# Kernel optimization log

Measured on AMD Instinct MI355X. Metric: run time of the kernel, lower is better.

Reference implementation:

```python
import jax, jax.numpy as jnp
import numpy as np

N_NODES = 50000
N_FRAMES = 5
N_EDGES = 400000
H1, C1 = 8, 8
D_MODEL = 64
N_HEADS, HEAD_DIM = 4, 16
EPS = 1e-5


def _gat_conv(h_in, src, dst, W, a_src, a_dst, heads, ch):
    # PyG GATConv (eval mode): linear -> per-head attn logits -> leaky_relu ->
    # segment softmax over incoming edges of each dst node -> weighted scatter-add.
    N = h_in.shape[0]
    h = (h_in @ W.T).reshape(N, heads, ch)            # [N,H,C]
    a_s = (h * a_src).sum(-1)                          # [N,H]
    a_d = (h * a_dst).sum(-1)                          # [N,H]
    e = jax.nn.leaky_relu(a_s[src] + a_d[dst], negative_slope=0.2)  # [E,H]
    e_max = jax.ops.segment_max(e, dst, num_segments=N)             # [N,H]
    ex = jnp.exp(e - e_max[dst])
    denom = jax.ops.segment_sum(ex, dst, num_segments=N)
    alpha = ex / denom[dst]                            # [E,H]
    return jax.ops.segment_sum(h[src] * alpha[..., None], dst, num_segments=N)  # [N,H,C]


def _ln(x, w, b):
    m = x.mean(-1, keepdims=True)
    v = ((x - m) ** 2).mean(-1, keepdims=True)
    return (x - m) / jnp.sqrt(v + EPS) * w + b


def _forward(x, edge_index, W1, att_src1, att_dst1, b1, W2, att_src2, att_dst2, b2,
             tWqkv, tbqkv, tWo, tbo, tln1w, tln1b, tWff1, tbff1, tWff2, tbff2,
             tln2w, tln2b, Wh1, bh1, Wh2, bh2):
    loops = jnp.arange(N_NODES, dtype=edge_index.dtype)  # add_self_loops=True
    embs = []
    for f in range(N_FRAMES):  # fixed small frame window
        src = jnp.concatenate([edge_index[f, 0], loops])
        dst = jnp.concatenate([edge_index[f, 1], loops])
        h = _gat_conv(x[f], src, dst, W1, att_src1, att_dst1, H1, C1).reshape(N_NODES, H1 * C1) + b1
        h = jax.nn.elu(h)
        h = _gat_conv(h, src, dst, W2, att_src2, att_dst2, 1, D_MODEL)[:, 0] + b2  # concat=False, 1 head
        embs.append(h.mean(0))  # graph embedding [64]
    seq = jnp.stack(embs)[None]  # [1,5,64]
    scale = 1.0 / np.sqrt(HEAD_DIM)
    for l in range(tWqkv.shape[0]):  # post-norm TransformerEncoderLayer (eval, relu)
        B, S, _ = seq.shape
        qkv = seq @ tWqkv[l].T + tbqkv[l]
        q, k, v = jnp.split(qkv, 3, axis=-1)
        q = q.reshape(B, S, N_HEADS, HEAD_DIM)
        k = k.reshape(B, S, N_HEADS, HEAD_DIM)
        v = v.reshape(B, S, N_HEADS, HEAD_DIM)
        att = jax.nn.softmax(jnp.einsum('bqhd,bkhd->bhqk', q, k) * scale, axis=-1)
        o = jnp.einsum('bhqk,bkhd->bqhd', att, v).reshape(B, S, D_MODEL)
        seq = _ln(seq + o @ tWo[l].T + tbo[l], tln1w[l], tln1b[l])
        ff = jax.nn.relu(seq @ tWff1[l].T + tbff1[l]) @ tWff2[l].T + tbff2[l]
        seq = _ln(seq + ff, tln2w[l], tln2b[l])
    last = seq[:, -1, :]
    return jax.nn.relu(last @ Wh1.T + bh1) @ Wh2.T + bh2  # [1,2]


def setup_inputs():
    key = jax.random.key(0)
    ks = jax.random.split(key, 16)
    p = lambda i, shape, s=0.1: jax.random.normal(ks[i], shape, dtype=jnp.float32) * s
    return {
        'x': jax.random.normal(ks[0], (N_FRAMES, N_NODES, 13), dtype=jnp.float32),
        'edge_index': jax.random.randint(ks[1], (N_FRAMES, 2, N_EDGES), 0, N_NODES, dtype=jnp.int32),
        'W1': p(2, (64, 13)), 'att_src1': p(3, (H1, C1)), 'att_dst1': p(4, (H1, C1)), 'b1': jnp.zeros((64,), jnp.float32),
        'W2': p(5, (64, 64)), 'att_src2': p(6, (1, 64)), 'att_dst2': p(7, (1, 64)), 'b2': jnp.zeros((64,), jnp.float32),
        'tWqkv': p(8, (3, 192, 64)), 'tbqkv': jnp.zeros((3, 192), jnp.float32),
        'tWo': p(9, (3, 64, 64)), 'tbo': jnp.zeros((3, 64), jnp.float32),
        'tln1w': jnp.ones((3, 64), jnp.float32), 'tln1b': jnp.zeros((3, 64), jnp.float32),
        'tWff1': p(10, (3, 128, 64)), 'tbff1': jnp.zeros((3, 128), jnp.float32),
        'tWff2': p(11, (3, 64, 128)), 'tbff2': jnp.zeros((3, 64), jnp.float32),
        'tln2w': jnp.ones((3, 64), jnp.float32), 'tln2b': jnp.zeros((3, 64), jnp.float32),
        'Wh1': p(12, (32, 64)), 'bh1': jnp.zeros((32,), jnp.float32),
        'Wh2': p(13, (2, 32)), 'bh2': jnp.zeros((2,), jnp.float32),
    }


def reference(x, edge_index, W1, att_src1, att_dst1, b1, W2, att_src2, att_dst2, b2,
              tWqkv, tbqkv, tWo, tbo, tln1w, tln1b, tWff1, tbff1, tWff2, tbff2,
              tln2w, tln2b, Wh1, bh1, Wh2, bh2):
    return _forward(x, edge_index, W1, att_src1, att_dst1, b1, W2, att_src2, att_dst2, b2,
                    tWqkv, tbqkv, tWo, tbo, tln1w, tln1b, tWff1, tbff1, tWff2, tbff2,
                    tln2w, tln2b, Wh1, bh1, Wh2, bh2)
```

## Files before the change

### kernel.cpp

```cpp
#include <hip/hip_runtime.h>
#include <math.h>

#define NN_F 50000
#define NE_F 400000
#define BPF  768

__device__ __forceinline__ float lrelu02(float x) { return x > 0.f ? x : 0.2f * x; }
__device__ __forceinline__ float fexp(float x) { return __expf(x); }

__device__ __forceinline__ unsigned short f2bf(float f) {
  unsigned int u = __float_as_uint(f);
  u += 0x7fffu + ((u >> 16) & 1u);
  return (unsigned short)(u >> 16);
}
__device__ __forceinline__ float bf_lo(unsigned int u) { return __uint_as_float(u << 16); }
__device__ __forceinline__ float bf_hi(unsigned int u) { return __uint_as_float(u & 0xffff0000u); }
__device__ __forceinline__ unsigned int pack2(float a, float b) {
  return (unsigned int)f2bf(a) | ((unsigned int)f2bf(b) << 16);
}

typedef __attribute__((ext_vector_type(8))) short bfrag_t;
typedef __attribute__((ext_vector_type(4))) float facc_t;

__global__ void __launch_bounds__(256, 3)
k_rank_node1(const int* __restrict__ ei, int* __restrict__ deg,
             unsigned short* __restrict__ rank, int nFrames, int rankBlocks,
             const float* __restrict__ x, const float* __restrict__ W1,
             const float* __restrict__ attS, const float* __restrict__ attD,
             unsigned short* __restrict__ h1b, float* __restrict__ as1,
             float* __restrict__ ad1, int nNodes, int node1Blocks) {
  __shared__ float xbuf[4][16];
  if (blockIdx.x < rankBlocks) {
    int tid = blockIdx.x * blockDim.x + threadIdx.x;
    int T = (nFrames * NE_F) >> 2;
    if (tid >= T) return;
    int gd[4];
#pragma unroll
    for (int i = 0; i < 4; i++) {
      int e = tid + i * T;
      int f = e / NE_F, idx = e - f * NE_F;
      gd[i] = f * NN_F + ei[(size_t)f * 2 * NE_F + NE_F + idx];
    }
    int r[4];
#pragma unroll
    for (int i = 0; i < 4; i++) r[i] = atomicAdd(&deg[gd[i]], 1);
#pragma unroll
    for (int i = 0; i < 4; i++) rank[tid + i * T] = (unsigned short)r[i];
    return;
  }
  int bid = blockIdx.x - rankBlocks;
  int l = threadIdx.x & 63;
  int w = threadIdx.x >> 6;
  int wid = (bid * blockDim.x + threadIdx.x) >> 6;
  int nw = (node1Blocks * blockDim.x) >> 6;
  float4 wA = make_float4(W1[l * 13 + 0], W1[l * 13 + 1], W1[l * 13 + 2], W1[l * 13 + 3]);
  float4 wB = make_float4(W1[l * 13 + 4], W1[l * 13 + 5], W1[l * 13 + 6], W1[l * 13 + 7]);
  float4 wC = make_float4(W1[l * 13 + 8], W1[l * 13 + 9], W1[l * 13 + 10], W1[l * 13 + 11]);
  float4 wD = make_float4(W1[l * 13 + 12], 0.f, 0.f, 0.f);
  float aS = attS[l], aD = attD[l];
  const float4* xb = reinterpret_cast<const float4*>(xbuf[w]);
  for (int n = wid; n < nNodes; n += nw) {
    if (l < 16) xbuf[w][l] = (l < 13) ? x[(size_t)n * 13 + l] : 0.f;
    float4 x0 = xb[0], x1 = xb[1], x2 = xb[2], x3 = xb[3];
    float a0 = x0.x * wA.x, a1 = x0.y * wA.y, a2 = x0.z * wA.z, a3 = x0.w * wA.w;
    a0 = fmaf(x1.x, wB.x, a0); a1 = fmaf(x1.y, wB.y, a1);
    a2 = fmaf(x1.z, wB.z, a2); a3 = fmaf(x1.w, wB.w, a3);
    a0 = fmaf(x2.x, wC.x, a0); a1 = fmaf(x2.y, wC.y, a1);
    a2 = fmaf(x2.z, wC.z, a2); a3 = fmaf(x2.w, wC.w, a3);
    a0 = fmaf(x3.x, wD.x, a0);
    float acc = (a0 + a1) + (a2 + a3);
    h1b[(size_t)n * 64 + l] = f2bf(acc);
    float s = acc * aS, d = acc * aD;
#pragma unroll
    for (int off = 1; off < 8; off <<= 1) {
      s += __shfl_xor(s, off, 64);
      d += __shfl_xor(d, off, 64);
    }
    if ((l & 7) == 0) { as1[n * 8 + (l >> 3)] = s; ad1[n * 8 + (l >> 3)] = d; }
  }
}

__global__ void k_scan1(const int* __restrict__ deg, int* __restrict__ bsum, int nNodes) {
  __shared__ int part[256];
  int t = threadIdx.x;
  int i = blockIdx.x * 256 + t;
  part[t] = (i < nNodes) ? deg[i] : 0;
  __syncthreads();
  for (int off = 128; off > 0; off >>= 1) {
    if (t < off) part[t] += part[t + off];
    __syncthreads();
  }
  if (t == 0) bsum[blockIdx.x] = part[0];
}

__global__ void __launch_bounds__(1024)
k_scan2(const int* __restrict__ bsum, int* __restrict__ boff, int nblk) {
  __shared__ int part[1024];
  int t = threadIdx.x;
  part[t] = (t < nblk) ? bsum[t] : 0;
  __syncthreads();
  for (int off = 1; off < 1024; off <<= 1) {
    int v = (t >= off) ? part[t - off] : 0;
    __syncthreads();
    part[t] += v;
    __syncthreads();
  }
  if (t < nblk) boff[t] = part[t] - bsum[t];
}

__global__ void k_scan3(const int* __restrict__ deg, const int* __restrict__ boff,
                        int* __restrict__ rowptr, int nNodes, int nEdges) {
  __shared__ int part[256];
  int t = threadIdx.x;
  int i = blockIdx.x * 256 + t;
  int d = (i < nNodes) ? deg[i] : 0;
  part[t] = d;
  __syncthreads();
  for (int off = 1; off < 256; off <<= 1) {
    int v = (t >= off) ? part[t - off] : 0;
    __syncthreads();
    part[t] += v;
    __syncthreads();
  }
  if (i < nNodes) rowptr[i] = boff[blockIdx.x] + part[t] - d;
  if (blockIdx.x == 0 && t == 0) rowptr[nNodes] = nEdges;
}

__global__ void k_place(const int* __restrict__ ei, const int* __restrict__ rowptr,
                        const unsigned short* __restrict__ rank, int* __restrict__ csr,
                        int nFrames) {
  int tid = blockIdx.x * blockDim.x + threadIdx.x;
  int T = (nFrames * NE_F) >> 2;
  if (tid >= T) return;
#pragma unroll
  for (int i = 0; i < 4; i++) {
    int e = tid + i * T;
    int f = e / NE_F, idx = e - f * NE_F;
    const int* base = ei + (size_t)f * 2 * NE_F;
    int src = base[idx], dst = base[NE_F + idx];
    csr[rowptr[f * NN_F + dst] + (int)rank[e]] = f * NN_F + src;
  }
}

__global__ void __launch_bounds__(256)
k_agg1(const int* __restrict__ rowptr, const int* __restrict__ csr,
       const unsigned short* __restrict__ h1b, const float* __restrict__ as1,
       const float* __restrict__ ad1, unsigned short* __restrict__ out1b, int nNodes) {
  int t = threadIdx.x;
  int l = t & 63;
  int grp = l >> 3, q = l & 7;
  int n = ((blockIdx.x * blockDim.x + t) >> 6) * 8 + grp;
  if (n >= nNodes) return;
  float adv = ad1[n * 8 + q];
  float e0 = fexp(lrelu02(as1[n * 8 + q] + adv));
  uint4 pv = *reinterpret_cast<const uint4*>(h1b + (size_t)n * 64 + q * 8);
  float a0 = e0 * bf_lo(pv.x), a1 = e0 * bf_hi(pv.x);
  float a2 = e0 * bf_lo(pv.y), a3 = e0 * bf_hi(pv.y);
  float a4 = e0 * bf_lo(pv.z), a5 = e0 * bf_hi(pv.z);
  float a6 = e0 * bf_lo(pv.w), a7 = e0 * bf_hi(pv.w);
  float den = e0;
  int s0 = rowptr[n], s1 = rowptr[n + 1];
  int i = s0;
  for (; i + 2 <= s1; i += 2) {
    int src0 = csr[i], src1 = csr[i + 1];
    float ea = fexp(lrelu02(as1[src0 * 8 + q] + adv));
    float eb = fexp(lrelu02(as1[src1 * 8 + q] + adv));
    uint4 va = *reinterpret_cast<const uint4*>(h1b + (size_t)src0 * 64 + q * 8);
    uint4 vb = *reinterpret_cast<const uint4*>(h1b + (size_t)src1 * 64 + q * 8);
    a0 = fmaf(ea, bf_lo(va.x), a0); a1 = fmaf(ea, bf_hi(va.x), a1);
    a2 = fmaf(ea, bf_lo(va.y), a2); a3 = fmaf(ea, bf_hi(va.y), a3);
    a4 = fmaf(ea, bf_lo(va.z), a4); a5 = fmaf(ea, bf_hi(va.z), a5);
    a6 = fmaf(ea, bf_lo(va.w), a6); a7 = fmaf(ea, bf_hi(va.w), a7);
    a0 = fmaf(eb, bf_lo(vb.x), a0); a1 = fmaf(eb, bf_hi(vb.x), a1);
    a2 = fmaf(eb, bf_lo(vb.y), a2); a3 = fmaf(eb, bf_hi(vb.y), a3);
    a4 = fmaf(eb, bf_lo(vb.z), a4); a5 = fmaf(eb, bf_hi(vb.z), a5);
    a6 = fmaf(eb, bf_lo(vb.w), a6); a7 = fmaf(eb, bf_hi(vb.w), a7);
    den += ea + eb;
  }
  if (i < s1) {
    int src = csr[i];
    float e2 = fexp(lrelu02(as1[src * 8 + q] + adv));
    uint4 v = *reinterpret_cast<const uint4*>(h1b + (size_t)src * 64 + q * 8);
    a0 = fmaf(e2, bf_lo(v.x), a0); a1 = fmaf(e2, bf_hi(v.x), a1);
    a2 = fmaf(e2, bf_lo(v.y), a2); a3 = fmaf(e2, bf_hi(v.y), a3);
    a4 = fmaf(e2, bf_lo(v.z), a4); a5 = fmaf(e2, bf_hi(v.z), a5);
    a6 = fmaf(e2, bf_lo(v.w), a6); a7 = fmaf(e2, bf_hi(v.w), a7);
    den += e2;
  }
  float inv = 1.f / den;
  uint4 o;
  o.x = pack2(a0 * inv, a1 * inv);
  o.y = pack2(a2 * inv, a3 * inv);
  o.z = pack2(a4 * inv, a5 * inv);
  o.w = pack2(a6 * inv, a7 * inv);
  *reinterpret_cast<uint4*>(out1b + (size_t)n * 64 + q * 8) = o;
}

__global__ void __launch_bounds__(256)
k_node2(const unsigned short* __restrict__ out1b, const float* __restrict__ b1,
        const float* __restrict__ W2, const float* __restrict__ attS2,
        const float* __restrict__ attD2, unsigned short* __restrict__ gb,
        float* __restrict__ as2, float* __restrict__ ad2, int nNodes) {
  __shared__ unsigned short lg[4][16][72];
  int t = threadIdx.x, l = t & 63, w = t >> 6;
  int r16 = l & 15, g4 = l >> 4;

  bfrag_t bfr[8];
#pragma unroll
  for (int tt = 0; tt < 4; tt++) {
    const float* wrow = W2 + (tt * 16 + r16) * 64;
#pragma unroll
    for (int kc = 0; kc < 2; kc++) {
      float4 lo = *reinterpret_cast<const float4*>(wrow + kc * 32 + 4 * g4);
      float4 hi = *reinterpret_cast<const float4*>(wrow + kc * 32 + 16 + 4 * g4);
      union { unsigned short u[8]; bfrag_t v; } pk;
      pk.u[0] = f2bf(lo.x); pk.u[1] = f2bf(lo.y); pk.u[2] = f2bf(lo.z); pk.u[3] = f2bf(lo.w);
      pk.u[4] = f2bf(hi.x); pk.u[5] = f2bf(hi.y); pk.u[6] = f2bf(hi.z); pk.u[7] = f2bf(hi.w);
      bfr[tt * 2 + kc] = pk.v;
    }
  }
  float4 bias[2][2];
#pragma unroll
  for (int kc = 0; kc < 2; kc++)
#pragma unroll
    for (int h = 0; h < 2; h++)
      bias[kc][h] = *reinterpret_cast<const float4*>(b1 + kc * 32 + h * 16 + 4 * g4);
  float aSr0 = attS2[r16], aSr1 = attS2[16 + r16], aSr2 = attS2[32 + r16], aSr3 = attS2[48 + r16];
  float aDr0 = attD2[r16], aDr1 = attD2[16 + r16], aDr2 = attD2[32 + r16], aDr3 = attD2[48 + r16];

  int wid = (blockIdx.x * blockDim.x + t) >> 6;
  int nw = (gridDim.x * blockDim.x) >> 6;
  int ntiles = nNodes >> 4;
  for (int tile = wid; tile < ntiles; tile += nw) {
    int n0 = tile << 4;
    const unsigned short* arow = out1b + (size_t)(n0 + r16) * 64;
    facc_t acc0 = 0, acc1 = 0, acc2 = 0, acc3 = 0;
#pragma unroll
    for (int kc = 0; kc < 2; kc++) {
      union { unsigned short u[8]; bfrag_t v; } apk;
#pragma unroll
      for (int h = 0; h < 2; h++) {
        uint2 raw = *reinterpret_cast<const uint2*>(arow + kc * 32 + h * 16 + 4 * g4);
        float4 bb = bias[kc][h];
        float f0 = bf_lo(raw.x) + bb.x, f1 = bf_hi(raw.x) + bb.y;
        float f2 = bf_lo(raw.y) + bb.z, f3 = bf_hi(raw.y) + bb.w;
        f0 = f0 > 0.f ? f0 : (fexp(f0) - 1.f);
        f1 = f1 > 0.f ? f1 : (fexp(f1) - 1.f);
        f2 = f2 > 0.f ? f2 : (fexp(f2) - 1.f);
        f3 = f3 > 0.f ? f3 : (fexp(f3) - 1.f);
        apk.u[h * 4 + 0] = f2bf(f0); apk.u[h * 4 + 1] = f2bf(f1);
        apk.u[h * 4 + 2] = f2bf(f2); apk.u[h * 4 + 3] = f2bf(f3);
      }
      bfrag_t afr = apk.v;
      acc0 = __builtin_amdgcn_mfma_f32_16x16x32_bf16(afr, bfr[0 * 2 + kc], acc0, 0, 0, 0);
      acc1 = __builtin_amdgcn_mfma_f32_16x16x32_bf16(afr, bfr[1 * 2 + kc], acc1, 0, 0, 0);
      acc2 = __builtin_amdgcn_mfma_f32_16x16x32_bf16(afr, bfr[2 * 2 + kc], acc2, 0, 0, 0);
      acc3 = __builtin_amdgcn_mfma_f32_16x16x32_bf16(afr, bfr[3 * 2 + kc], acc3, 0, 0, 0);
    }
    float ps0 = acc0[0] * aSr0 + acc1[0] * aSr1 + acc2[0] * aSr2 + acc3[0] * aSr3;
    float ps1 = acc0[1] * aSr0 + acc1[1] * aSr1 + acc2[1] * aSr2 + acc3[1] * aSr3;
    float ps2 = acc0[2] * aSr0 + acc1[2] * aSr1 + acc2[2] * aSr2 + acc3[2] * aSr3;
    float ps3 = acc0[3] * aSr0 + acc1[3] * aSr1 + acc2[3] * aSr2 + acc3[3] * aSr3;
    float pd0 = acc0[0] * aDr0 + acc1[0] * aDr1 + acc2[0] * aDr2 + acc3[0] * aDr3;
    float pd1 = acc0[1] * aDr0 + acc1[1] * aDr1 + acc2[1] * aDr2 + acc3[1] * aDr3;
    float pd2 = acc0[2] * aDr0 + acc1[2] * aDr1 + acc2[2] * aDr2 + acc3[2] * aDr3;
    float pd3 = acc0[3] * aDr0 + acc1[3] * aDr1 + acc2[3] * aDr2 + acc3[3] * aDr3;
#pragma unroll
    for (int off = 1; off < 16; off <<= 1) {
      ps0 += __shfl_xor(ps0, off, 64); ps1 += __shfl_xor(ps1, off, 64);
      ps2 += __shfl_xor(ps2, off, 64); ps3 += __shfl_xor(ps3, off, 64);
      pd0 += __shfl_xor(pd0, off, 64); pd1 += __shfl_xor(pd1, off, 64);
      pd2 += __shfl_xor(pd2, off, 64); pd3 += __shfl_xor(pd3, off, 64);
    }
    if (r16 == 0) {
      *reinterpret_cast<float4*>(as2 + n0 + g4 * 4) = make_float4(ps0, ps1, ps2, ps3);
      *reinterpret_cast<float4*>(ad2 + n0 + g4 * 4) = make_float4(pd0, pd1, pd2, pd3);
    }
#pragma unroll
    for (int r = 0; r < 4; r++) {
      lg[w][g4 * 4 + r][0 * 16 + r16] = f2bf(acc0[r]);
      lg[w][g4 * 4 + r][1 * 16 + r16] = f2bf(acc1[r]);
      lg[w][g4 * 4 + r][2 * 16 + r16] = f2bf(acc2[r]);
      lg[w][g4 * 4 + r][3 * 16 + r16] = f2bf(acc3[r]);
    }
    asm volatile("s_waitcnt lgkmcnt(0)" ::: "memory");
    int row = l >> 3, c = l & 7;
    uint4 v0 = *reinterpret_cast<const uint4*>(&lg[w][row][c * 8]);
    uint4 v1 = *reinterpret_cast<const uint4*>(&lg[w][8 + row][c * 8]);
    *reinterpret_cast<uint4*>(gb + (size_t)(n0 + row) * 64 + c * 8) = v0;
    *reinterpret_cast<uint4*>(gb + (size_t)(n0 + 8 + row) * 64 + c * 8) = v1;
  }
}

__global__ void __launch_bounds__(256)
k_agg2mean(const int* __restrict__ rowptr, const int* __restrict__ csr,
           const unsigned short* __restrict__ gtab, const float* __restrict__ as2,
           const float* __restrict__ ad2, float* __restrict__ emb) {
  __shared__ float part[32][64];
  int t = threadIdx.x;
  int w = t >> 6, l = t & 63;
  int grp = l >> 3, q = l & 7;
  int f = blockIdx.x / BPF;
  int gf = (blockIdx.x - f * BPF) * 32 + w * 8 + grp;
  const int stride = BPF * 32;
  float m0 = 0.f, m1 = 0.f, m2 = 0.f, m3 = 0.f, m4 = 0.f, m5 = 0.f, m6 = 0.f, m7 = 0.f;
  for (int j = gf; j < NN_F; j += stride) {
    int n = f * NN_F + j;
    float adv = ad2[n];
    float e0 = fexp(lrelu02(as2[n] + adv));
    uint4 pv = *reinterpret_cast<const uint4*>(gtab + (size_t)n * 64 + q * 8);
    float a0 = e0 * bf_lo(pv.x), a1 = e0 * bf_hi(pv.x);
    float a2 = e0 * bf_lo(pv.y), a3 = e0 * bf_hi(pv.y);
    float a4 = e0 * bf_lo(pv.z), a5 = e0 * bf_hi(pv.z);
    float a6 = e0 * bf_lo(pv.w), a7 = e0 * bf_hi(pv.w);
    float den = e0;
    int s0 = rowptr[n], s1 = rowptr[n + 1];
    int i = s0;
    for (; i + 2 <= s1; i += 2) {
      int src0 = csr[i], src1 = csr[i + 1];
      float ea = fexp(lrelu02(as2[src0] + adv));
      float eb = fexp(lrelu02(as2[src1] + adv));
      uint4 va = *reinterpret_cast<const uint4*>(gtab + (size_t)src0 * 64 + q * 8);
      uint4 vb = *reinterpret_cast<const uint4*>(gtab + (size_t)src1 * 64 + q * 8);
      a0 = fmaf(ea, bf_lo(va.x), a0); a1 = fmaf(ea, bf_hi(va.x), a1);
      a2 = fmaf(ea, bf_lo(va.y), a2); a3 = fmaf(ea, bf_hi(va.y), a3);
      a4 = fmaf(ea, bf_lo(va.z), a4); a5 = fmaf(ea, bf_hi(va.z), a5);
      a6 = fmaf(ea, bf_lo(va.w), a6); a7 = fmaf(ea, bf_hi(va.w), a7);
      a0 = fmaf(eb, bf_lo(vb.x), a0); a1 = fmaf(eb, bf_hi(vb.x), a1);
      a2 = fmaf(eb, bf_lo(vb.y), a2); a3 = fmaf(eb, bf_hi(vb.y), a3);
      a4 = fmaf(eb, bf_lo(vb.z), a4); a5 = fmaf(eb, bf_hi(vb.z), a5);
      a6 = fmaf(eb, bf_lo(vb.w), a6); a7 = fmaf(eb, bf_hi(vb.w), a7);
      den += ea + eb;
    }
    if (i < s1) {
      int src = csr[i];
      float e2 = fexp(lrelu02(as2[src] + adv));
      uint4 v = *reinterpret_cast<const uint4*>(gtab + (size_t)src * 64 + q * 8);
      a0 = fmaf(e2, bf_lo(v.x), a0); a1 = fmaf(e2, bf_hi(v.x), a1);
      a2 = fmaf(e2, bf_lo(v.y), a2); a3 = fmaf(e2, bf_hi(v.y), a3);
      a4 = fmaf(e2, bf_lo(v.z), a4); a5 = fmaf(e2, bf_hi(v.z), a5);
      a6 = fmaf(e2, bf_lo(v.w), a6); a7 = fmaf(e2, bf_hi(v.w), a7);
      den += e2;
    }
    float inv = 1.f / den;
    m0 = fmaf(a0, inv, m0); m1 = fmaf(a1, inv, m1);
    m2 = fmaf(a2, inv, m2); m3 = fmaf(a3, inv, m3);
    m4 = fmaf(a4, inv, m4); m5 = fmaf(a5, inv, m5);
    m6 = fmaf(a6, inv, m6); m7 = fmaf(a7, inv, m7);
  }
  float4* pr = reinterpret_cast<float4*>(&part[w * 8 + grp][q * 8]);
  pr[0] = make_float4(m0, m1, m2, m3);
  pr[1] = make_float4(m4, m5, m6, m7);
  __syncthreads();
  if (t < 64) {
    float s = 0.f;
#pragma unroll
    for (int r = 0; r < 32; r++) s += part[r][t];
    atomicAdd(&emb[f * 64 + t], s * (1.0f / NN_F));
  }
}

__device__ __forceinline__ float grp16_reduce(float p) {
#pragma unroll
  for (int off = 1; off < 16; off <<= 1) p += __shfl_xor(p, off, 64);
  return p;
}

__global__ void __launch_bounds__(1024)
k_transformer(const float* __restrict__ emb, const float* __restrict__ b2,
              const float* __restrict__ Wqkv, const float* __restrict__ bqkv,
              const float* __restrict__ Wo, const float* __restrict__ bo,
              const float* __restrict__ ln1w, const float* __restrict__ ln1b,
              const float* __restrict__ Wff1, const float* __restrict__ bff1,
              const float* __restrict__ Wff2, const float* __restrict__ bff2,
              const float* __restrict__ ln2w, const float* __restrict__ ln2b,
              const float* __restrict__ Wh1, const float* __restrict__ bh1,
              const float* __restrict__ Wh2, const float* __restrict__ bh2,
              float* __restrict__ out) {
  __shared__ float seq[5][64];
  __shared__ float qkv[5][192];
  __shared__ float att[4][5][5];
  __shared__ float aob[5][64];
  __shared__ float ffb[5][128];
  __shared__ float tmp[5][64];
  __shared__ float hid[32];
  int t = threadIdx.x;
  int l = t & 63, w = t >> 6;
  int g = l >> 4, q = l & 15;

  if (t < 320) seq[t >> 6][t & 63] = emb[t] + b2[t & 63];
  __syncthreads();

  for (int ly = 0; ly < 3; ly++) {
    const float* Wq  = Wqkv + ly * 12288; const float* bq  = bqkv + ly * 192;
    const float* Wol = Wo   + ly * 4096;  const float* bol = bo   + ly * 64;
    const float* w1  = ln1w + ly * 64;    const float* bb1 = ln1b + ly * 64;
    const float* Wf1 = Wff1 + ly * 8192;  const float* bf1 = bff1 + ly * 128;
    const float* Wf2 = Wff2 + ly * 8192;  const float* bf2 = bff2 + ly * 64;
    const float* w2  = ln2w + ly * 64;    const float* bb2 = ln2b + ly * 64;

    for (int o = w * 4 + g; o < 960; o += 64) {
      int s = o / 192, j = o - s * 192;
      float4 wv = *reinterpret_cast<const float4*>(&Wq[j * 64 + q * 4]);
      float4 xv = *reinterpret_cast<const float4*>(&seq[s][q * 4]);
      float p = wv.x * xv.x + wv.y * xv.y + wv.z * xv.z + wv.w * xv.w;
      p = grp16_reduce(p);
      if (q == 0) qkv[s][j] = p + bq[j];
    }
    __syncthreads();

    if (t < 100) {
      int hh = t / 25, qs = (t / 5) % 5, ks = t % 5;
      float acc = 0.f;
      for (int d = 0; d < 16; d++)
        acc = fmaf(qkv[qs][hh * 16 + d], qkv[ks][64 + hh * 16 + d], acc);
      att[hh][qs][ks] = acc * 0.25f;
    }
    __syncthreads();
    if (t < 20) {
      int hh = t / 5, qs = t % 5;
      float m = att[hh][qs][0];
      for (int k2 = 1; k2 < 5; k2++) m = fmaxf(m, att[hh][qs][k2]);
      float ss = 0.f;
      for (int k2 = 0; k2 < 5; k2++) { float v = expf(att[hh][qs][k2] - m); att[hh][qs][k2] = v; ss += v; }
      float inv = 1.f / ss;
      for (int k2 = 0; k2 < 5; k2++) att[hh][qs][k2] *= inv;
    }
    __syncthreads();

    if (t < 320) {
      int s = t >> 6, j = t & 63, hh = j >> 4;
      float acc = 0.f;
      for (int k2 = 0; k2 < 5; k2++) acc = fmaf(att[hh][s][k2], qkv[k2][128 + j], acc);
      aob[s][j] = acc;
    }
    __syncthreads();

    for (int o = w * 4 + g; o < 320; o += 64) {
      int s = o >> 6, c = o & 63;
      float4 wv = *reinterpret_cast<const float4*>(&Wol[c * 64 + q * 4]);
      float4 xv = *reinterpret_cast<const float4*>(&aob[s][q * 4]);
      float p = wv.x * xv.x + wv.y * xv.y + wv.z * xv.z + wv.w * xv.w;
      p = grp16_reduce(p);
      if (q == 0) tmp[s][c] = seq[s][c] + p + bol[c];
    }
    __syncthreads();

    if (w < 5) {
      float v = tmp[w][l];
      float s1 = v, s2 = v * v;
#pragma unroll
      for (int off = 1; off < 64; off <<= 1) {
        s1 += __shfl_xor(s1, off, 64);
        s2 += __shfl_xor(s2, off, 64);
      }
      float m = s1 * (1.f / 64.f);
      float var = s2 * (1.f / 64.f) - m * m;
      float inv = 1.f / sqrtf(var + 1e-5f);
      seq[w][l] = (v - m) * inv * w1[l] + bb1[l];
    }
    __syncthreads();

    for (int o = w * 4 + g; o < 640; o += 64) {
      int s = o >> 7, j = o & 127;
      float4 wv = *reinterpret_cast<const float4*>(&Wf1[j * 64 + q * 4]);
      float4 xv = *reinterpret_cast<const float4*>(&seq[s][q * 4]);
      float p = wv.x * xv.x + wv.y * xv.y + wv.z * xv.z + wv.w * xv.w;
      p = grp16_reduce(p);
      if (q == 0) ffb[s][j] = fmaxf(p + bf1[j], 0.f);
    }
    __syncthreads();

    for (int o = w * 4 + g; o < 320; o += 64) {
      int s = o >> 6, c = o & 63;
      float4 wa = *reinterpret_cast<const float4*>(&Wf2[c * 128 + q * 8]);
      float4 wb = *reinterpret_cast<const float4*>(&Wf2[c * 128 + q * 8 + 4]);
      float4 xa = *reinterpret_cast<const float4*>(&ffb[s][q * 8]);
      float4 xb = *reinterpret_cast<const float4*>(&ffb[s][q * 8 + 4]);
      float p = wa.x * xa.x + wa.y * xa.y + wa.z * xa.z + wa.w * xa.w
              + wb.x * xb.x + wb.y * xb.y + wb.z * xb.z + wb.w * xb.w;
      p = grp16_reduce(p);
      if (q == 0) tmp[s][c] = seq[s][c] + p + bf2[c];
    }
    __syncthreads();

    if (w < 5) {
      float v = tmp[w][l];
      float s1 = v, s2 = v * v;
#pragma unroll
      for (int off = 1; off < 64; off <<= 1) {
        s1 += __shfl_xor(s1, off, 64);
        s2 += __shfl_xor(s2, off, 64);
      }
      float m = s1 * (1.f / 64.f);
      float var = s2 * (1.f / 64.f) - m * m;
      float inv = 1.f / sqrtf(var + 1e-5f);
      seq[w][l] = (v - m) * inv * w2[l] + bb2[l];
    }
    __syncthreads();
  }

  for (int o = w * 4 + g; o < 32; o += 64) {
    float4 wv = *reinterpret_cast<const float4*>(&Wh1[o * 64 + q * 4]);
    float4 xv = *reinterpret_cast<const float4*>(&seq[4][q * 4]);
    float p = wv.x * xv.x + wv.y * xv.y + wv.z * xv.z + wv.w * xv.w;
    p = grp16_reduce(p);
    if (q == 0) hid[o] = fmaxf(p + bh1[o], 0.f);
  }
  __syncthreads();
  if (t < 2) {
    float acc = bh2[t];
    for (int j = 0; j < 32; j++) acc = fmaf(hid[j], Wh2[t * 32 + j], acc);
    out[t] = acc;
  }
}

extern "C" void kernel_launch(void* const* d_in, const int* in_sizes, int n_in,
                              void* d_out, int out_size, void* d_ws, size_t ws_size,
                              hipStream_t stream) {
  const float* x     = (const float*)d_in[0];
  const int*   ei    = (const int*)d_in[1];
  const float* W1    = (const float*)d_in[2];
  const float* attS1 = (const float*)d_in[3];
  const float* attD1 = (const float*)d_in[4];
  const float* b1    = (const float*)d_in[5];
  const float* W2    = (const float*)d_in[6];
  const float* attS2 = (const float*)d_in[7];
  const float* attD2 = (const float*)d_in[8];
  const float* b2    = (const float*)d_in[9];
  const float* tWqkv = (const float*)d_in[10];
  const float* tbqkv = (const float*)d_in[11];
  const float* tWo   = (const float*)d_in[12];
  const float* tbo   = (const float*)d_in[13];
  const float* tln1w = (const float*)d_in[14];
  const float* tln1b = (const float*)d_in[15];
  const float* tWff1 = (const float*)d_in[16];
  const float* tbff1 = (const float*)d_in[17];
  const float* tWff2 = (const float*)d_in[18];
  const float* tbff2 = (const float*)d_in[19];
  const float* tln2w = (const float*)d_in[20];
  const float* tln2b = (const float*)d_in[21];
  const float* Wh1   = (const float*)d_in[22];
  const float* bh1   = (const float*)d_in[23];
  const float* Wh2   = (const float*)d_in[24];
  const float* bh2   = (const float*)d_in[25];
  float* out = (float*)d_out;

  auto need_bytes = [](int F) -> size_t {
    size_t NT = (size_t)F * NN_F, ET = (size_t)F * NE_F;
    return (NT * 18 + 320) * 4 + (NT * 192 + ET) * 2 + (NT * 2 + 1 + 2048 + ET) * 4;
  };
  const int F = (ws_size >= need_bytes(5)) ? 5 : 1;
  const int NT = F * NN_F, ET = F * NE_F;

  float* ws  = (float*)d_ws;
  float* as1 = ws;
  float* ad1 = as1 + (size_t)NT * 8;
  float* as2 = ad1 + (size_t)NT * 8;
  float* ad2 = as2 + NT;
  float* emb = ad2 + NT;
  unsigned short* h1b   = (unsigned short*)(emb + 320);
  unsigned short* gb    = h1b + (size_t)NT * 64;
  unsigned short* out1b = gb + (size_t)NT * 64;
  int* deg    = (int*)(out1b + (size_t)NT * 64);
  int* rowptr = deg + NT;
  int* bsum   = rowptr + NT + 1;
  int* boff   = bsum + 1024;
  unsigned short* rank = (unsigned short*)(boff + 1024);
  int* csr    = (int*)(rank + ET);

  (void)hipMemsetAsync(emb, 0, 320 * sizeof(float), stream);

  const int nblk = (NT + 255) / 256;
  const int edge4Blocks = ((ET >> 2) + 255) / 256;
  const int agg1Blocks = (NT / 8 + 3) / 4;
  const int node1Blocks = 2048;
  const int node2Blocks = 1024;

  for (int f0 = 0; f0 < 5; f0 += F) {
    const float* xf = x + (size_t)f0 * NN_F * 13;
    const int* eif  = ei + (size_t)f0 * 2 * NE_F;

    (void)hipMemsetAsync(deg, 0, NT * sizeof(int), stream);
    k_rank_node1<<<edge4Blocks + node1Blocks, 256, 0, stream>>>(
        eif, deg, rank, F, edge4Blocks,
        xf, W1, attS1, attD1, h1b, as1, ad1, NT, node1Blocks);
    k_scan1<<<nblk, 256, 0, stream>>>(deg, bsum, NT);
    k_scan2<<<1, 1024, 0, stream>>>(bsum, boff, nblk);
    k_scan3<<<nblk, 256, 0, stream>>>(deg, boff, rowptr, NT, ET);
    k_place<<<edge4Blocks, 256, 0, stream>>>(eif, rowptr, rank, csr, F);

    k_agg1<<<agg1Blocks, 256, 0, stream>>>(rowptr, csr, h1b, as1, ad1, out1b, NT);
    k_node2<<<node2Blocks, 256, 0, stream>>>(out1b, b1, W2, attS2, attD2, gb, as2, ad2, NT);
    k_agg2mean<<<F * BPF, 256, 0, stream>>>(rowptr, csr, gb, as2, ad2, emb + f0 * 64);
  }

  k_transformer<<<1, 1024, 0, stream>>>(emb, b2, tWqkv, tbqkv, tWo, tbo, tln1w, tln1b,
                                        tWff1, tbff1, tWff2, tbff2, tln2w, tln2b,
                                        Wh1, bh1, Wh2, bh2, out);
}
```

Before: 360.5 us.

## Fuse layer-1 aggregation with layer-2 linear via LDS and unroll edge loops by four

Merges the first GAT aggregation kernel with the second layer's linear/attention projection kernel. Each block aggregates 32 nodes, applies the bias and ELU, stages the bf16 rows in shared memory, and then two waves run the MFMA projection, so the out1b buffer no longer round-trips through global memory and one launch is dropped. The edge gather loops in both aggregation kernels are also unrolled from two to four edges to put more loads in flight. In exchange, only two of the four waves do the MFMA stage, every chunk needs two block barriers, and the larger unroll raises register pressure.

```diff
diff --git a/kernel.cpp b/kernel.cpp
--- a/kernel.cpp
+++ b/kernel.cpp
@@ -142,67 +142,58 @@
   }
 }
 
+#define EDGE_ACC(tab, srcv, attarr, attidx)                          \
+  {                                                                  \
+    float e2 = fexp(lrelu02(attarr[attidx] + adv));                  \
+    uint4 v = *reinterpret_cast<const uint4*>(tab + (size_t)(srcv) * 64 + q * 8); \
+    a0 = fmaf(e2, bf_lo(v.x), a0); a1 = fmaf(e2, bf_hi(v.x), a1);    \
+    a2 = fmaf(e2, bf_lo(v.y), a2); a3 = fmaf(e2, bf_hi(v.y), a3);    \
+    a4 = fmaf(e2, bf_lo(v.z), a4); a5 = fmaf(e2, bf_hi(v.z), a5);    \
+    a6 = fmaf(e2, bf_lo(v.w), a6); a7 = fmaf(e2, bf_hi(v.w), a7);    \
+    den += e2;                                                       \
+  }
+
+#define EDGE_LOOP4(tab, attexpr_a, attexpr_b, attexpr_c, attexpr_d)  \
+  for (; i + 4 <= s1; i += 4) {                                      \
+    int sa = csr[i], sb = csr[i + 1], sc = csr[i + 2], sd = csr[i + 3]; \
+    float ea = fexp(lrelu02((attexpr_a) + adv));                     \
+    float eb = fexp(lrelu02((attexpr_b) + adv));                     \
+    float ec = fexp(lrelu02((attexpr_c) + adv));                     \
+    float ed = fexp(lrelu02((attexpr_d) + adv));                     \
+    uint4 va = *reinterpret_cast<const uint4*>(tab + (size_t)sa * 64 + q * 8); \
+    uint4 vb = *reinterpret_cast<const uint4*>(tab + (size_t)sb * 64 + q * 8); \
+    uint4 vc = *reinterpret_cast<const uint4*>(tab + (size_t)sc * 64 + q * 8); \
+    uint4 vd = *reinterpret_cast<const uint4*>(tab + (size_t)sd * 64 + q * 8); \
+    a0 = fmaf(ea, bf_lo(va.x), a0); a1 = fmaf(ea, bf_hi(va.x), a1);  \
+    a2 = fmaf(ea, bf_lo(va.y), a2); a3 = fmaf(ea, bf_hi(va.y), a3);  \
+    a4 = fmaf(ea, bf_lo(va.z), a4); a5 = fmaf(ea, bf_hi(va.z), a5);  \
+    a6 = fmaf(ea, bf_lo(va.w), a6); a7 = fmaf(ea, bf_hi(va.w), a7);  \
+    a0 = fmaf(eb, bf_lo(vb.x), a0); a1 = fmaf(eb, bf_hi(vb.x), a1);  \
+    a2 = fmaf(eb, bf_lo(vb.y), a2); a3 = fmaf(eb, bf_hi(vb.y), a3);  \
+    a4 = fmaf(eb, bf_lo(vb.z), a4); a5 = fmaf(eb, bf_hi(vb.z), a5);  \
+    a6 = fmaf(eb, bf_lo(vb.w), a6); a7 = fmaf(eb, bf_hi(vb.w), a7);  \
+    a0 = fmaf(ec, bf_lo(vc.x), a0); a1 = fmaf(ec, bf_hi(vc.x), a1);  \
+    a2 = fmaf(ec, bf_lo(vc.y), a2); a3 = fmaf(ec, bf_hi(vc.y), a3);  \
+    a4 = fmaf(ec, bf_lo(vc.z), a4); a5 = fmaf(ec, bf_hi(vc.z), a5);  \
+    a6 = fmaf(ec, bf_lo(vc.w), a6); a7 = fmaf(ec, bf_hi(vc.w), a7);  \
+    a0 = fmaf(ed, bf_lo(vd.x), a0); a1 = fmaf(ed, bf_hi(vd.x), a1);  \
+    a2 = fmaf(ed, bf_lo(vd.y), a2); a3 = fmaf(ed, bf_hi(vd.y), a3);  \
+    a4 = fmaf(ed, bf_lo(vd.z), a4); a5 = fmaf(ed, bf_hi(vd.z), a5);  \
+    a6 = fmaf(ed, bf_lo(vd.w), a6); a7 = fmaf(ed, bf_hi(vd.w), a7);  \
+    den += (ea + eb) + (ec + ed);                                    \
+  }
+
 __global__ void __launch_bounds__(256)
-k_agg1(const int* __restrict__ rowptr, const int* __restrict__ csr,
-       const unsigned short* __restrict__ h1b, const float* __restrict__ as1,
-       const float* __restrict__ ad1, unsigned short* __restrict__ out1b, int nNodes) {
-  int t = threadIdx.x;
-  int l = t & 63;
+k_agg1node2(const int* __restrict__ rowptr, const int* __restrict__ csr,
+            const unsigned short* __restrict__ h1b, const float* __restrict__ as1,
+            const float* __restrict__ ad1, const float* __restrict__ b1,
+            const float* __restrict__ W2, const float* __restrict__ attS2,
+            const float* __restrict__ attD2, unsigned short* __restrict__ gb,
+            float* __restrict__ as2, float* __restrict__ ad2, int nNodes) {
+  __shared__ unsigned short lout[32][68];
+  __shared__ unsigned short lg[2][16][72];
+  int t = threadIdx.x, l = t & 63, w = t >> 6;
   int grp = l >> 3, q = l & 7;
-  int n = ((blockIdx.x * blockDim.x + t) >> 6) * 8 + grp;
-  if (n >= nNodes) return;
-  float adv = ad1[n * 8 + q];
-  float e0 = fexp(lrelu02(as1[n * 8 + q] + adv));
-  uint4 pv = *reinterpret_cast<const uint4*>(h1b + (size_t)n * 64 + q * 8);
-  float a0 = e0 * bf_lo(pv.x), a1 = e0 * bf_hi(pv.x);
-  float a2 = e0 * bf_lo(pv.y), a3 = e0 * bf_hi(pv.y);
-  float a4 = e0 * bf_lo(pv.z), a5 = e0 * bf_hi(pv.z);
-  float a6 = e0 * bf_lo(pv.w), a7 = e0 * bf_hi(pv.w);
-  float den = e0;
-  int s0 = rowptr[n], s1 = rowptr[n + 1];
-  int i = s0;
-  for (; i + 2 <= s1; i += 2) {
-    int src0 = csr[i], src1 = csr[i + 1];
-    float ea = fexp(lrelu02(as1[src0 * 8 + q] + adv));
-    float eb = fexp(lrelu02(as1[src1 * 8 + q] + adv));
-    uint4 va = *reinterpret_cast<const uint4*>(h1b + (size_t)src0 * 64 + q * 8);
-    uint4 vb = *reinterpret_cast<const uint4*>(h1b + (size_t)src1 * 64 + q * 8);
-    a0 = fmaf(ea, bf_lo(va.x), a0); a1 = fmaf(ea, bf_hi(va.x), a1);
-    a2 = fmaf(ea, bf_lo(va.y), a2); a3 = fmaf(ea, bf_hi(va.y), a3);
-    a4 = fmaf(ea, bf_lo(va.z), a4); a5 = fmaf(ea, bf_hi(va.z), a5);
-    a6 = fmaf(ea, bf_lo(va.w), a6); a7 = fmaf(ea, bf_hi(va.w), a7);
-    a0 = fmaf(eb, bf_lo(vb.x), a0); a1 = fmaf(eb, bf_hi(vb.x), a1);
-    a2 = fmaf(eb, bf_lo(vb.y), a2); a3 = fmaf(eb, bf_hi(vb.y), a3);
-    a4 = fmaf(eb, bf_lo(vb.z), a4); a5 = fmaf(eb, bf_hi(vb.z), a5);
-    a6 = fmaf(eb, bf_lo(vb.w), a6); a7 = fmaf(eb, bf_hi(vb.w), a7);
-    den += ea + eb;
-  }
-  if (i < s1) {
-    int src = csr[i];
-    float e2 = fexp(lrelu02(as1[src * 8 + q] + adv));
-    uint4 v = *reinterpret_cast<const uint4*>(h1b + (size_t)src * 64 + q * 8);
-    a0 = fmaf(e2, bf_lo(v.x), a0); a1 = fmaf(e2, bf_hi(v.x), a1);
-    a2 = fmaf(e2, bf_lo(v.y), a2); a3 = fmaf(e2, bf_hi(v.y), a3);
-    a4 = fmaf(e2, bf_lo(v.z), a4); a5 = fmaf(e2, bf_hi(v.z), a5);
-    a6 = fmaf(e2, bf_lo(v.w), a6); a7 = fmaf(e2, bf_hi(v.w), a7);
-    den += e2;
-  }
-  float inv = 1.f / den;
-  uint4 o;
-  o.x = pack2(a0 * inv, a1 * inv);
-  o.y = pack2(a2 * inv, a3 * inv);
-  o.z = pack2(a4 * inv, a5 * inv);
-  o.w = pack2(a6 * inv, a7 * inv);
-  *reinterpret_cast<uint4*>(out1b + (size_t)n * 64 + q * 8) = o;
-}
-
-__global__ void __launch_bounds__(256)
-k_node2(const unsigned short* __restrict__ out1b, const float* __restrict__ b1,
-        const float* __restrict__ W2, const float* __restrict__ attS2,
-        const float* __restrict__ attD2, unsigned short* __restrict__ gb,
-        float* __restrict__ as2, float* __restrict__ ad2, int nNodes) {
-  __shared__ unsigned short lg[4][16][72];
-  int t = threadIdx.x, l = t & 63, w = t >> 6;
   int r16 = l & 15, g4 = l >> 4;
 
   bfrag_t bfr[8];
@@ -219,76 +210,99 @@
       bfr[tt * 2 + kc] = pk.v;
     }
   }
-  float4 bias[2][2];
-#pragma unroll
-  for (int kc = 0; kc < 2; kc++)
-#pragma unroll
-    for (int h = 0; h < 2; h++)
-      bias[kc][h] = *reinterpret_cast<const float4*>(b1 + kc * 32 + h * 16 + 4 * g4);
+  float4 bA = *reinterpret_cast<const float4*>(b1 + q * 8);
+  float4 bB = *reinterpret_cast<const float4*>(b1 + q * 8 + 4);
   float aSr0 = attS2[r16], aSr1 = attS2[16 + r16], aSr2 = attS2[32 + r16], aSr3 = attS2[48 + r16];
   float aDr0 = attD2[r16], aDr1 = attD2[16 + r16], aDr2 = attD2[32 + r16], aDr3 = attD2[48 + r16];
 
-  int wid = (blockIdx.x * blockDim.x + t) >> 6;
-  int nw = (gridDim.x * blockDim.x) >> 6;
-  int ntiles = nNodes >> 4;
-  for (int tile = wid; tile < ntiles; tile += nw) {
-    int n0 = tile << 4;
-    const unsigned short* arow = out1b + (size_t)(n0 + r16) * 64;
-    facc_t acc0 = 0, acc1 = 0, acc2 = 0, acc3 = 0;
-#pragma unroll
-    for (int kc = 0; kc < 2; kc++) {
-      union { unsigned short u[8]; bfrag_t v; } apk;
-#pragma unroll
-      for (int h = 0; h < 2; h++) {
-        uint2 raw = *reinterpret_cast<const uint2*>(arow + kc * 32 + h * 16 + 4 * g4);
-        float4 bb = bias[kc][h];
-        float f0 = bf_lo(raw.x) + bb.x, f1 = bf_hi(raw.x) + bb.y;
-        float f2 = bf_lo(raw.y) + bb.z, f3 = bf_hi(raw.y) + bb.w;
-        f0 = f0 > 0.f ? f0 : (fexp(f0) - 1.f);
-        f1 = f1 > 0.f ? f1 : (fexp(f1) - 1.f);
-        f2 = f2 > 0.f ? f2 : (fexp(f2) - 1.f);
-        f3 = f3 > 0.f ? f3 : (fexp(f3) - 1.f);
-        apk.u[h * 4 + 0] = f2bf(f0); apk.u[h * 4 + 1] = f2bf(f1);
-        apk.u[h * 4 + 2] = f2bf(f2); apk.u[h * 4 + 3] = f2bf(f3);
-      }
-      bfrag_t afr = apk.v;
-      acc0 = __builtin_amdgcn_mfma_f32_16x16x32_bf16(afr, bfr[0 * 2 + kc], acc0, 0, 0, 0);
-      acc1 = __builtin_amdgcn_mfma_f32_16x16x32_bf16(afr, bfr[1 * 2 + kc], acc1, 0, 0, 0);
-      acc2 = __builtin_amdgcn_mfma_f32_16x16x32_bf16(afr, bfr[2 * 2 + kc], acc2, 0, 0, 0);
-      acc3 = __builtin_amdgcn_mfma_f32_16x16x32_bf16(afr, bfr[3 * 2 + kc], acc3, 0, 0, 0);
-    }
-    float ps0 = acc0[0] * aSr0 + acc1[0] * aSr1 + acc2[0] * aSr2 + acc3[0] * aSr3;
-    float ps1 = acc0[1] * aSr0 + acc1[1] * aSr1 + acc2[1] * aSr2 + acc3[1] * aSr3;
-    float ps2 = acc0[2] * aSr0 + acc1[2] * aSr1 + acc2[2] * aSr2 + acc3[2] * aSr3;
-    float ps3 = acc0[3] * aSr0 + acc1[3] * aSr1 + acc2[3] * aSr2 + acc3[3] * aSr3;
-    float pd0 = acc0[0] * aDr0 + acc1[0] * aDr1 + acc2[0] * aDr2 + acc3[0] * aDr3;
-    float pd1 = acc0[1] * aDr0 + acc1[1] * aDr1 + acc2[1] * aDr2 + acc3[1] * aDr3;
-    float pd2 = acc0[2] * aDr0 + acc1[2] * aDr1 + acc2[2] * aDr2 + acc3[2] * aDr3;
-    float pd3 = acc0[3] * aDr0 + acc1[3] * aDr1 + acc2[3] * aDr2 + acc3[3] * aDr3;
-#pragma unroll
-    for (int off = 1; off < 16; off <<= 1) {
-      ps0 += __shfl_xor(ps0, off, 64); ps1 += __shfl_xor(ps1, off, 64);
-      ps2 += __shfl_xor(ps2, off, 64); ps3 += __shfl_xor(ps3, off, 64);
-      pd0 += __shfl_xor(pd0, off, 64); pd1 += __shfl_xor(pd1, off, 64);
-      pd2 += __shfl_xor(pd2, off, 64); pd3 += __shfl_xor(pd3, off, 64);
-    }
-    if (r16 == 0) {
-      *reinterpret_cast<float4*>(as2 + n0 + g4 * 4) = make_float4(ps0, ps1, ps2, ps3);
-      *reinterpret_cast<float4*>(ad2 + n0 + g4 * 4) = make_float4(pd0, pd1, pd2, pd3);
-    }
-#pragma unroll
-    for (int r = 0; r < 4; r++) {
-      lg[w][g4 * 4 + r][0 * 16 + r16] = f2bf(acc0[r]);
-      lg[w][g4 * 4 + r][1 * 16 + r16] = f2bf(acc1[r]);
-      lg[w][g4 * 4 + r][2 * 16 + r16] = f2bf(acc2[r]);
-      lg[w][g4 * 4 + r][3 * 16 + r16] = f2bf(acc3[r]);
-    }
-    asm volatile("s_waitcnt lgkmcnt(0)" ::: "memory");
-    int row = l >> 3, c = l & 7;
-    uint4 v0 = *reinterpret_cast<const uint4*>(&lg[w][row][c * 8]);
-    uint4 v1 = *reinterpret_cast<const uint4*>(&lg[w][8 + row][c * 8]);
-    *reinterpret_cast<uint4*>(gb + (size_t)(n0 + row) * 64 + c * 8) = v0;
-    *reinterpret_cast<uint4*>(gb + (size_t)(n0 + 8 + row) * 64 + c * 8) = v1;
+  int nchunks = (nNodes + 31) >> 5;
+  for (int c = blockIdx.x; c < nchunks; c += gridDim.x) {
+    int n0 = c << 5;
+    int n = n0 + w * 8 + grp;
+    if (n < nNodes) {
+      float adv = ad1[n * 8 + q];
+      float e0 = fexp(lrelu02(as1[n * 8 + q] + adv));
+      uint4 pv = *reinterpret_cast<const uint4*>(h1b + (size_t)n * 64 + q * 8);
+      float a0 = e0 * bf_lo(pv.x), a1 = e0 * bf_hi(pv.x);
+      float a2 = e0 * bf_lo(pv.y), a3 = e0 * bf_hi(pv.y);
+      float a4 = e0 * bf_lo(pv.z), a5 = e0 * bf_hi(pv.z);
+      float a6 = e0 * bf_lo(pv.w), a7 = e0 * bf_hi(pv.w);
+      float den = e0;
+      int s0 = rowptr[n], s1 = rowptr[n + 1];
+      int i = s0;
+      EDGE_LOOP4(h1b, as1[sa * 8 + q], as1[sb * 8 + q], as1[sc * 8 + q], as1[sd * 8 + q])
+      for (; i < s1; i++) {
+        int src = csr[i];
+        EDGE_ACC(h1b, src, as1, src * 8 + q)
+      }
+      float inv = 1.f / den;
+      float h0 = a0 * inv + bA.x, h1 = a1 * inv + bA.y;
+      float h2 = a2 * inv + bA.z, h3 = a3 * inv + bA.w;
+      float h4 = a4 * inv + bB.x, h5 = a5 * inv + bB.y;
+      float h6 = a6 * inv + bB.z, h7 = a7 * inv + bB.w;
+      h0 = h0 > 0.f ? h0 : (fexp(h0) - 1.f);
+      h1 = h1 > 0.f ? h1 : (fexp(h1) - 1.f);
+      h2 = h2 > 0.f ? h2 : (fexp(h2) - 1.f);
+      h3 = h3 > 0.f ? h3 : (fexp(h3) - 1.f);
+      h4 = h4 > 0.f ? h4 : (fexp(h4) - 1.f);
+      h5 = h5 > 0.f ? h5 : (fexp(h5) - 1.f);
+      h6 = h6 > 0.f ? h6 : (fexp(h6) - 1.f);
+      h7 = h7 > 0.f ? h7 : (fexp(h7) - 1.f);
+      uint4 o;
+      o.x = pack2(h0, h1); o.y = pack2(h2, h3);
+      o.z = pack2(h4, h5); o.w = pack2(h6, h7);
+      *reinterpret_cast<uint4*>(&lout[w * 8 + grp][q * 8]) = o;
+    }
+    __syncthreads();
+    int tb = n0 + w * 16;
+    if (w < 2 && tb < nNodes) {
+      const unsigned short* arow = &lout[w * 16 + r16][0];
+      facc_t acc0 = 0, acc1 = 0, acc2 = 0, acc3 = 0;
+#pragma unroll
+      for (int kc = 0; kc < 2; kc++) {
+        union { uint2 d[2]; bfrag_t v; } apk;
+        apk.d[0] = *reinterpret_cast<const uint2*>(arow + kc * 32 + 4 * g4);
+        apk.d[1] = *reinterpret_cast<const uint2*>(arow + kc * 32 + 16 + 4 * g4);
+        bfrag_t afr = apk.v;
+        acc0 = __builtin_amdgcn_mfma_f32_16x16x32_bf16(afr, bfr[0 * 2 + kc], acc0, 0, 0, 0);
+        acc1 = __builtin_amdgcn_mfma_f32_16x16x32_bf16(afr, bfr[1 * 2 + kc], acc1, 0, 0, 0);
+        acc2 = __builtin_amdgcn_mfma_f32_16x16x32_bf16(afr, bfr[2 * 2 + kc], acc2, 0, 0, 0);
+        acc3 = __builtin_amdgcn_mfma_f32_16x16x32_bf16(afr, bfr[3 * 2 + kc], acc3, 0, 0, 0);
+      }
+      float ps0 = acc0[0] * aSr0 + acc1[0] * aSr1 + acc2[0] * aSr2 + acc3[0] * aSr3;
+      float ps1 = acc0[1] * aSr0 + acc1[1] * aSr1 + acc2[1] * aSr2 + acc3[1] * aSr3;
+      float ps2 = acc0[2] * aSr0 + acc1[2] * aSr1 + acc2[2] * aSr2 + acc3[2] * aSr3;
+      float ps3 = acc0[3] * aSr0 + acc1[3] * aSr1 + acc2[3] * aSr2 + acc3[3] * aSr3;
+      float pd0 = acc0[0] * aDr0 + acc1[0] * aDr1 + acc2[0] * aDr2 + acc3[0] * aDr3;
+      float pd1 = acc0[1] * aDr0 + acc1[1] * aDr1 + acc2[1] * aDr2 + acc3[1] * aDr3;
+      float pd2 = acc0[2] * aDr0 + acc1[2] * aDr1 + acc2[2] * aDr2 + acc3[2] * aDr3;
+      float pd3 = acc0[3] * aDr0 + acc1[3] * aDr1 + acc2[3] * aDr2 + acc3[3] * aDr3;
+#pragma unroll
+      for (int off = 1; off < 16; off <<= 1) {
+        ps0 += __shfl_xor(ps0, off, 64); ps1 += __shfl_xor(ps1, off, 64);
+        ps2 += __shfl_xor(ps2, off, 64); ps3 += __shfl_xor(ps3, off, 64);
+        pd0 += __shfl_xor(pd0, off, 64); pd1 += __shfl_xor(pd1, off, 64);
+        pd2 += __shfl_xor(pd2, off, 64); pd3 += __shfl_xor(pd3, off, 64);
+      }
+      if (r16 == 0) {
+        *reinterpret_cast<float4*>(as2 + tb + g4 * 4) = make_float4(ps0, ps1, ps2, ps3);
+        *reinterpret_cast<float4*>(ad2 + tb + g4 * 4) = make_float4(pd0, pd1, pd2, pd3);
+      }
+#pragma unroll
+      for (int r = 0; r < 4; r++) {
+        lg[w][g4 * 4 + r][0 * 16 + r16] = f2bf(acc0[r]);
+        lg[w][g4 * 4 + r][1 * 16 + r16] = f2bf(acc1[r]);
+        lg[w][g4 * 4 + r][2 * 16 + r16] = f2bf(acc2[r]);
+        lg[w][g4 * 4 + r][3 * 16 + r16] = f2bf(acc3[r]);
+      }
+      asm volatile("s_waitcnt lgkmcnt(0)" ::: "memory");
+      int row = l >> 3, cc = l & 7;
+      uint4 v0 = *reinterpret_cast<const uint4*>(&lg[w][row][cc * 8]);
+      uint4 v1 = *reinterpret_cast<const uint4*>(&lg[w][8 + row][cc * 8]);
+      *reinterpret_cast<uint4*>(gb + (size_t)(tb + row) * 64 + cc * 8) = v0;
+      *reinterpret_cast<uint4*>(gb + (size_t)(tb + 8 + row) * 64 + cc * 8) = v1;
+    }
+    __syncthreads();
   }
 }
 
@@ -316,31 +330,10 @@
     float den = e0;
     int s0 = rowptr[n], s1 = rowptr[n + 1];
     int i = s0;
-    for (; i + 2 <= s1; i += 2) {
-      int src0 = csr[i], src1 = csr[i + 1];
-      float ea = fexp(lrelu02(as2[src0] + adv));
-      float eb = fexp(lrelu02(as2[src1] + adv));
-      uint4 va = *reinterpret_cast<const uint4*>(gtab + (size_t)src0 * 64 + q * 8);
-      uint4 vb = *reinterpret_cast<const uint4*>(gtab + (size_t)src1 * 64 + q * 8);
-      a0 = fmaf(ea, bf_lo(va.x), a0); a1 = fmaf(ea, bf_hi(va.x), a1);
-      a2 = fmaf(ea, bf_lo(va.y), a2); a3 = fmaf(ea, bf_hi(va.y), a3);
-      a4 = fmaf(ea, bf_lo(va.z), a4); a5 = fmaf(ea, bf_hi(va.z), a5);
-      a6 = fmaf(ea, bf_lo(va.w), a6); a7 = fmaf(ea, bf_hi(va.w), a7);
-      a0 = fmaf(eb, bf_lo(vb.x), a0); a1 = fmaf(eb, bf_hi(vb.x), a1);
-      a2 = fmaf(eb, bf_lo(vb.y), a2); a3 = fmaf(eb, bf_hi(vb.y), a3);
-      a4 = fmaf(eb, bf_lo(vb.z), a4); a5 = fmaf(eb, bf_hi(vb.z), a5);
-      a6 = fmaf(eb, bf_lo(vb.w), a6); a7 = fmaf(eb, bf_hi(vb.w), a7);
-      den += ea + eb;
-    }
-    if (i < s1) {
+    EDGE_LOOP4(gtab, as2[sa], as2[sb], as2[sc], as2[sd])
+    for (; i < s1; i++) {
       int src = csr[i];
-      float e2 = fexp(lrelu02(as2[src] + adv));
-      uint4 v = *reinterpret_cast<const uint4*>(gtab + (size_t)src * 64 + q * 8);
-      a0 = fmaf(e2, bf_lo(v.x), a0); a1 = fmaf(e2, bf_hi(v.x), a1);
-      a2 = fmaf(e2, bf_lo(v.y), a2); a3 = fmaf(e2, bf_hi(v.y), a3);
-      a4 = fmaf(e2, bf_lo(v.z), a4); a5 = fmaf(e2, bf_hi(v.z), a5);
-      a6 = fmaf(e2, bf_lo(v.w), a6); a7 = fmaf(e2, bf_hi(v.w), a7);
-      den += e2;
+      EDGE_ACC(gtab, src, as2, src)
     }
     float inv = 1.f / den;
     m0 = fmaf(a0, inv, m0); m1 = fmaf(a1, inv, m1);
@@ -548,7 +541,7 @@
 
   auto need_bytes = [](int F) -> size_t {
     size_t NT = (size_t)F * NN_F, ET = (size_t)F * NE_F;
-    return (NT * 18 + 320) * 4 + (NT * 192 + ET) * 2 + (NT * 2 + 1 + 2048 + ET) * 4;
+    return (NT * 18 + 320) * 4 + (NT * 128 + ET) * 2 + (NT * 2 + 1 + 2048 + ET) * 4;
   };
   const int F = (ws_size >= need_bytes(5)) ? 5 : 1;
   const int NT = F * NN_F, ET = F * NE_F;
@@ -559,10 +552,9 @@
   float* as2 = ad1 + (size_t)NT * 8;
   float* ad2 = as2 + NT;
   float* emb = ad2 + NT;
-  unsigned short* h1b   = (unsigned short*)(emb + 320);
-  unsigned short* gb    = h1b + (size_t)NT * 64;
-  unsigned short* out1b = gb + (size_t)NT * 64;
-  int* deg    = (int*)(out1b + (size_t)NT * 64);
+  unsigned short* h1b = (unsigned short*)(emb + 320);
+  unsigned short* gb  = h1b + (size_t)NT * 64;
+  int* deg    = (int*)(gb + (size_t)NT * 64);
   int* rowptr = deg + NT;
   int* bsum   = rowptr + NT + 1;
   int* boff   = bsum + 1024;
@@ -573,9 +565,8 @@
 
   const int nblk = (NT + 255) / 256;
   const int edge4Blocks = ((ET >> 2) + 255) / 256;
-  const int agg1Blocks = (NT / 8 + 3) / 4;
   const int node1Blocks = 2048;
-  const int node2Blocks = 1024;
+  const int aggFusedBlocks = 2048;
 
   for (int f0 = 0; f0 < 5; f0 += F) {
     const float* xf = x + (size_t)f0 * NN_F * 13;
@@ -590,8 +581,8 @@
     k_scan3<<<nblk, 256, 0, stream>>>(deg, boff, rowptr, NT, ET);
     k_place<<<edge4Blocks, 256, 0, stream>>>(eif, rowptr, rank, csr, F);
 
-    k_agg1<<<agg1Blocks, 256, 0, stream>>>(rowptr, csr, h1b, as1, ad1, out1b, NT);
-    k_node2<<<node2Blocks, 256, 0, stream>>>(out1b, b1, W2, attS2, attD2, gb, as2, ad2, NT);
+    k_agg1node2<<<aggFusedBlocks, 256, 0, stream>>>(
+        rowptr, csr, h1b, as1, ad1, b1, W2, attS2, attD2, gb, as2, ad2, NT);
     k_agg2mean<<<F * BPF, 256, 0, stream>>>(rowptr, csr, gb, as2, ad2, emb + f0 * 64);
   }
 
```

New measurement: 409.8 us. +13.7%, slower.
